# Optimization experiments

Measured on AMD Instinct MI355X. Metric: run time of the kernel, lower is better.

Reference implementation:

```python
import jax, jax.numpy as jnp
import numpy as np

B, N, D, C, H = 16384, 32, 256, 128, 8
LEAKY_ALPHA = 0.2  # tf.nn.leaky_relu default


def setup_inputs() -> dict:
    key = jax.random.key(0)
    k1, k2, k3, k4 = jax.random.split(key, 4)
    return {
        "node_feats": jax.random.normal(k1, (B, D), dtype=jnp.float32),
        "neighbors_feats": jax.random.normal(k2, (B, N, D), dtype=jnp.float32),
        "kernel": jax.random.normal(k3, (D, C), dtype=jnp.float32) * 0.05,
        "attn_kernel": jax.random.normal(k4, (1, H, 2 * C), dtype=jnp.float32) * 0.05,
        "attn_bias": jnp.zeros((H * C,), dtype=jnp.float32),
    }


def reference(node_feats, neighbors_feats, kernel, attn_kernel, attn_bias):
    # Project node and neighbor features: [B,C], [B,N,C]
    node_p = jnp.einsum('bd,dc->bc', node_feats, kernel)
    neigh_p = jnp.einsum('bnd,dc->bnc', neighbors_feats, kernel)
    # attn_kernel [1,H,2C]: split instead of materializing tile+concat [B,N,2C]
    a = attn_kernel[0]                 # [H, 2C]
    a_src, a_dst = a[:, :C], a[:, C:]  # each [H, C]
    # score[b,n,h] = concat(node_p[b], neigh_p[b,n]) . a[h]
    scores = (jnp.einsum('bc,hc->bh', node_p, a_src)[:, None, :]
              + jnp.einsum('bnc,hc->bnh', neigh_p, a_dst))  # [B,N,H]
    scores = jnp.transpose(scores, (0, 2, 1))  # [B,H,N]
    coef = jax.nn.softmax(jax.nn.leaky_relu(scores, LEAKY_ALPHA), axis=-1)
    # dropout is identity at inference (Keras default training=False)
    z = jnp.einsum('bhn,bnc->bhc', coef, neigh_p)  # [B,H,C]
    z = z.reshape(B, H * C) + attn_bias            # concat heads + bias
    return z[None, ...]  # [1,B,H*C]
```

## Files before the change

### kernel.cpp

```cpp
#include <hip/hip_runtime.h>

#define BB 16384
#define NN 32
#define DD 256
#define CC 128
#define HH 8
#define ALPHA 0.2f

#define SA_STRIDE 264
#define SP_STRIDE 48

typedef __attribute__((ext_vector_type(8))) short bf16x8;
typedef __attribute__((ext_vector_type(4))) float f32x4;

__device__ __forceinline__ unsigned short f2b(float x) {
    unsigned int u = __float_as_uint(x);
    return (unsigned short)((u + 0x7fffu + ((u >> 16) & 1u)) >> 16);
}
__device__ __forceinline__ uint2 pack4(float a, float b, float c, float d) {
    uint2 r;
    r.x = (unsigned)f2b(a) | ((unsigned)f2b(b) << 16);
    r.y = (unsigned)f2b(c) | ((unsigned)f2b(d) << 16);
    return r;
}

__global__ __launch_bounds__(256) void prep_kernel(const float* __restrict__ kern,
                                                   const float* __restrict__ attn,
                                                   unsigned short* __restrict__ kfrag,
                                                   unsigned short* __restrict__ sfrag) {
    if (blockIdx.x < 16) {
        int tid = blockIdx.x * 256 + threadIdx.x;
        int nt   = tid >> 9;
        int ks   = (tid >> 6) & 7;
        int lane = tid & 63;
        int q    = lane >> 4;
        int cc   = lane & 15;
        int c    = nt * 16 + cc;
        unsigned short v[8];
#pragma unroll
        for (int j = 0; j < 8; ++j) {
            int k = ks * 32 + q * 8 + j;
            v[j] = f2b(kern[k * CC + c]);
        }
        uint4* dst = (uint4*)(kfrag + ((size_t)(nt * 8 + ks) * 64 + lane) * 8);
        uint4 pk;
        pk.x = (unsigned)v[0] | ((unsigned)v[1] << 16);
        pk.y = (unsigned)v[2] | ((unsigned)v[3] << 16);
        pk.z = (unsigned)v[4] | ((unsigned)v[5] << 16);
        pk.w = (unsigned)v[6] | ((unsigned)v[7] << 16);
        *dst = pk;
    } else {
        int sid = (blockIdx.x - 16) * 256 + threadIdx.x;
        int ks   = sid >> 6;
        int lane = sid & 63;
        int q    = lane >> 4;
        int cc   = lane & 15;
        unsigned short v[8];
#pragma unroll
        for (int j = 0; j < 8; ++j) {
            int k = ks * 32 + q * 8 + j;
            const float* krow = kern + (size_t)k * CC;
            const float* arow = (cc < 8) ? (attn + cc * (2 * CC) + CC)
                                         : (attn + (cc - 8) * (2 * CC));
            float s0 = 0.f, s1 = 0.f;
#pragma unroll 4
            for (int c = 0; c < CC; c += 2) {
                s0 += krow[c] * arow[c];
                s1 += krow[c + 1] * arow[c + 1];
            }
            v[j] = f2b(s0 + s1);
        }
        uint4* dst = (uint4*)(sfrag + ((size_t)ks * 64 + lane) * 8);
        uint4 pk;
        pk.x = (unsigned)v[0] | ((unsigned)v[1] << 16);
        pk.y = (unsigned)v[2] | ((unsigned)v[3] << 16);
        pk.z = (unsigned)v[4] | ((unsigned)v[5] << 16);
        pk.w = (unsigned)v[6] | ((unsigned)v[7] << 16);
        *dst = pk;
    }
}

__global__ __launch_bounds__(256, 4) void gat_kernel(const float* __restrict__ node,
                                                     const float* __restrict__ neigh,
                                                     const float* __restrict__ bias,
                                                     const unsigned short* __restrict__ kfrag,
                                                     const unsigned short* __restrict__ sfrag,
                                                     float* __restrict__ out) {
    const int b    = blockIdx.x;
    const int t    = threadIdx.x;
    const int lane = t & 63;
    const int wave = t >> 6;
    const int q    = lane >> 4;
    const int m15  = lane & 15;

    __shared__ __align__(16) char smem[39712];
    unsigned short* sA    = (unsigned short*)smem;
    unsigned short* sP    = (unsigned short*)(smem + 25344);
    unsigned short* cfrag = (unsigned short*)(smem + 37632);
    float*          sDst  = (float*)(smem + 38656);
    float*          sSrc  = (float*)(smem + 39680);

    {
        const float4* nb4 = (const float4*)(neigh + (size_t)b * (NN * DD));
        const float4* nd4 = (const float4*)(node + (size_t)b * DD);
        for (int j = t; j < 33 * 64; j += 256) {
            int row = j >> 6, d4 = j & 63;
            float4 v = (row < 32) ? nb4[row * 64 + d4] : nd4[d4];
            *(uint2*)(sA + row * SA_STRIDE + d4 * 4) = pack4(v.x, v.y, v.z, v.w);
        }
    }
    __syncthreads();

    if (wave < 3) {
        const int mt = wave;
        f32x4 acc = {0.f, 0.f, 0.f, 0.f};
        const unsigned short* abase = sA + (mt * 16 + m15) * SA_STRIDE + q * 8;
#pragma unroll
        for (int ks = 0; ks < 8; ++ks) {
            bf16x8 bfr = *(const bf16x8*)(sfrag + ((size_t)ks * 64 + lane) * 8);
            bf16x8 afr = *(const bf16x8*)(abase + ks * 32);
            acc = __builtin_amdgcn_mfma_f32_16x16x32_bf16(afr, bfr, acc, 0, 0, 0);
        }
#pragma unroll
        for (int r = 0; r < 4; ++r) {
            int row = mt * 16 + q * 4 + r;
            if (row < 32 && m15 < 8) sDst[row * 8 + m15] = acc[r];
            if (row == 32 && m15 >= 8) sSrc[m15 - 8] = acc[r];
        }
    }

#pragma unroll
    for (int nti = 0; nti < 2; ++nti) {
        const int nt = wave * 2 + nti;
        bf16x8 kb[8];
#pragma unroll
        for (int ks = 0; ks < 8; ++ks)
            kb[ks] = *(const bf16x8*)(kfrag + ((size_t)(nt * 8 + ks) * 64 + lane) * 8);
#pragma unroll
        for (int mt = 0; mt < 2; ++mt) {
            f32x4 acc = {0.f, 0.f, 0.f, 0.f};
            const unsigned short* abase = sA + (mt * 16 + m15) * SA_STRIDE + q * 8;
#pragma unroll
            for (int ks = 0; ks < 8; ++ks) {
                bf16x8 afr = *(const bf16x8*)(abase + ks * 32);
                acc = __builtin_amdgcn_mfma_f32_16x16x32_bf16(afr, kb[ks], acc, 0, 0, 0);
            }
            int c  = nt * 16 + m15;
            int n0 = mt * 16 + q * 4;
            *(uint2*)(sP + c * SP_STRIDE + n0) = pack4(acc[0], acc[1], acc[2], acc[3]);
        }
    }
    __syncthreads();

    {
        int h = t >> 5, n = t & 31;
        float sc = sSrc[h] + sDst[n * 8 + h];
        sc = fmaxf(sc, ALPHA * sc);
        float m = sc;
#pragma unroll
        for (int off = 16; off >= 1; off >>= 1) m = fmaxf(m, __shfl_xor(m, off, 32));
        float e = expf(sc - m);
        float den = e;
#pragma unroll
        for (int off = 16; off >= 1; off >>= 1) den += __shfl_xor(den, off, 32);
        float coef = e / den;
        int l1 = (n >> 3) * 16 + h;
        int jj = n & 7;
        cfrag[l1 * 8 + jj] = f2b(coef);
        cfrag[(l1 + 8) * 8 + jj] = 0;
    }
    __syncthreads();

    {
        bf16x8 cb = *(const bf16x8*)(cfrag + (size_t)lane * 8);
        f32x4 zero = {0.f, 0.f, 0.f, 0.f};
#pragma unroll
        for (int i = 0; i < 2; ++i) {
            int mt5 = wave * 2 + i;
            bf16x8 afr = *(const bf16x8*)(sP + (mt5 * 16 + m15) * SP_STRIDE + q * 8);
            f32x4 acc = __builtin_amdgcn_mfma_f32_16x16x32_bf16(afr, cb, zero, 0, 0, 0);
            if (m15 < 8) {
                int h  = m15;
                int c0 = mt5 * 16 + q * 4;
                float4 bv = *(const float4*)(bias + h * CC + c0);
                float4 r;
                r.x = acc[0] + bv.x;
                r.y = acc[1] + bv.y;
                r.z = acc[2] + bv.z;
                r.w = acc[3] + bv.w;
                *(float4*)(out + (size_t)b * (HH * CC) + h * CC + c0) = r;
            }
        }
    }
}

extern "C" void kernel_launch(void* const* d_in, const int* in_sizes, int n_in,
                              void* d_out, int out_size, void* d_ws, size_t ws_size,
                              hipStream_t stream) {
    const float* node  = (const float*)d_in[0];
    const float* neigh = (const float*)d_in[1];
    const float* kern  = (const float*)d_in[2];
    const float* attn  = (const float*)d_in[3];
    const float* bias  = (const float*)d_in[4];
    float* out = (float*)d_out;

    unsigned short* kfrag = (unsigned short*)d_ws;
    unsigned short* sfrag = (unsigned short*)((char*)d_ws + 65536);

    hipLaunchKernelGGL(prep_kernel, dim3(18), dim3(256), 0, stream, kern, attn, kfrag, sfrag);
    hipLaunchKernelGGL(gat_kernel, dim3(BB), dim3(256), 0, stream,
                       node, neigh, bias, kfrag, sfrag, out);
}
```

Measured before the change: 793.4 us.

## Make GAT blocks persistent over 8 batch rows with register-prefetched next-row loads

Each block now processes 8 consecutive batch rows instead of one, cutting the grid from one block per row to 2048 blocks. The next row's neighbor and node features are loaded into registers while the current row's projection, softmax and aggregation run, then written to shared memory after the projection buffer is no longer needed. This hides global load latency behind compute and amortizes per-block setup. In exchange it uses 36 extra VGPRs for the prefetch, drops the 4-blocks-per-CU launch bound, gives fewer blocks to schedule, and adds a padding change to the sP stride.

```diff
diff --git a/kernel.cpp b/kernel.cpp
--- a/kernel.cpp
+++ b/kernel.cpp
@@ -7,8 +7,18 @@
 #define HH 8
 #define ALPHA 0.2f
 
+#define GRID 2048
+#define NPB 8
+
 #define SA_STRIDE 264
-#define SP_STRIDE 48
+#define SP_STRIDE 56
+#define SA_BYTES (33 * SA_STRIDE * 2)
+#define SP_BYTES (CC * SP_STRIDE * 2)
+#define OFF_SP   SA_BYTES
+#define OFF_CF   (OFF_SP + SP_BYTES)
+#define OFF_DST  (OFF_CF + 1024)
+#define OFF_SRC  (OFF_DST + 1024)
+#define SMEM_TOT (OFF_SRC + 32)
 
 typedef __attribute__((ext_vector_type(8))) short bf16x8;
 typedef __attribute__((ext_vector_type(4))) float f32x4;
@@ -80,117 +90,164 @@
     }
 }
 
-__global__ __launch_bounds__(256, 4) void gat_kernel(const float* __restrict__ node,
-                                                     const float* __restrict__ neigh,
-                                                     const float* __restrict__ bias,
-                                                     const unsigned short* __restrict__ kfrag,
-                                                     const unsigned short* __restrict__ sfrag,
-                                                     float* __restrict__ out) {
-    const int b    = blockIdx.x;
+__global__ __launch_bounds__(256) void gat_kernel(const float* __restrict__ node,
+                                                  const float* __restrict__ neigh,
+                                                  const float* __restrict__ bias,
+                                                  const unsigned short* __restrict__ kfrag,
+                                                  const unsigned short* __restrict__ sfrag,
+                                                  float* __restrict__ out) {
     const int t    = threadIdx.x;
     const int lane = t & 63;
     const int wave = t >> 6;
     const int q    = lane >> 4;
     const int m15  = lane & 15;
 
-    __shared__ __align__(16) char smem[39712];
+    __shared__ __align__(16) char smem[SMEM_TOT];
     unsigned short* sA    = (unsigned short*)smem;
-    unsigned short* sP    = (unsigned short*)(smem + 25344);
-    unsigned short* cfrag = (unsigned short*)(smem + 37632);
-    float*          sDst  = (float*)(smem + 38656);
-    float*          sSrc  = (float*)(smem + 39680);
+    unsigned short* sP    = (unsigned short*)(smem + OFF_SP);
+    unsigned short* cfrag = (unsigned short*)(smem + OFF_CF);
+    float*          sDst  = (float*)(smem + OFF_DST);
+    float*          sSrc  = (float*)(smem + OFF_SRC);
+
+    const int base = blockIdx.x * NPB;
 
     {
-        const float4* nb4 = (const float4*)(neigh + (size_t)b * (NN * DD));
-        const float4* nd4 = (const float4*)(node + (size_t)b * DD);
-        for (int j = t; j < 33 * 64; j += 256) {
-            int row = j >> 6, d4 = j & 63;
-            float4 v = (row < 32) ? nb4[row * 64 + d4] : nd4[d4];
-            *(uint2*)(sA + row * SA_STRIDE + d4 * 4) = pack4(v.x, v.y, v.z, v.w);
+        int h = t >> 5, n = t & 31;
+        int l1 = (n >> 3) * 16 + h;
+        cfrag[(l1 + 8) * 8 + (n & 7)] = 0;
+    }
+
+    float4 r[9];
+
+    {
+        const float4* nb4 = (const float4*)(neigh + (size_t)base * (NN * DD));
+        const float4* nd4 = (const float4*)(node + (size_t)base * DD);
+#pragma unroll
+        for (int u = 0; u < 9; ++u) {
+            int j = t + (u << 8);
+            if (j < 33 * 64) {
+                int row = j >> 6, d4 = j & 63;
+                r[u] = (row < 32) ? nb4[row * 64 + d4] : nd4[d4];
+            }
+        }
+#pragma unroll
+        for (int u = 0; u < 9; ++u) {
+            int j = t + (u << 8);
+            if (j < 33 * 64) {
+                int row = j >> 6, d4 = j & 63;
+                *(uint2*)(sA + row * SA_STRIDE + d4 * 4) = pack4(r[u].x, r[u].y, r[u].z, r[u].w);
+            }
         }
     }
     __syncthreads();
 
-    if (wave < 3) {
-        const int mt = wave;
-        f32x4 acc = {0.f, 0.f, 0.f, 0.f};
-        const unsigned short* abase = sA + (mt * 16 + m15) * SA_STRIDE + q * 8;
-#pragma unroll
-        for (int ks = 0; ks < 8; ++ks) {
-            bf16x8 bfr = *(const bf16x8*)(sfrag + ((size_t)ks * 64 + lane) * 8);
-            bf16x8 afr = *(const bf16x8*)(abase + ks * 32);
-            acc = __builtin_amdgcn_mfma_f32_16x16x32_bf16(afr, bfr, acc, 0, 0, 0);
-        }
-#pragma unroll
-        for (int r = 0; r < 4; ++r) {
-            int row = mt * 16 + q * 4 + r;
-            if (row < 32 && m15 < 8) sDst[row * 8 + m15] = acc[r];
-            if (row == 32 && m15 >= 8) sSrc[m15 - 8] = acc[r];
-        }
-    }
-
-#pragma unroll
-    for (int nti = 0; nti < 2; ++nti) {
-        const int nt = wave * 2 + nti;
-        bf16x8 kb[8];
-#pragma unroll
-        for (int ks = 0; ks < 8; ++ks)
-            kb[ks] = *(const bf16x8*)(kfrag + ((size_t)(nt * 8 + ks) * 64 + lane) * 8);
-#pragma unroll
-        for (int mt = 0; mt < 2; ++mt) {
+    for (int i = 0; i < NPB; ++i) {
+        const int b = base + i;
+
+        if (i + 1 < NPB) {
+            const float4* nb4 = (const float4*)(neigh + (size_t)(b + 1) * (NN * DD));
+            const float4* nd4 = (const float4*)(node + (size_t)(b + 1) * DD);
+#pragma unroll
+            for (int u = 0; u < 9; ++u) {
+                int j = t + (u << 8);
+                if (j < 33 * 64) {
+                    int row = j >> 6, d4 = j & 63;
+                    r[u] = (row < 32) ? nb4[row * 64 + d4] : nd4[d4];
+                }
+            }
+        }
+
+        if (wave < 3) {
+            const int mt = wave;
             f32x4 acc = {0.f, 0.f, 0.f, 0.f};
             const unsigned short* abase = sA + (mt * 16 + m15) * SA_STRIDE + q * 8;
 #pragma unroll
             for (int ks = 0; ks < 8; ++ks) {
+                bf16x8 bfr = *(const bf16x8*)(sfrag + ((size_t)ks * 64 + lane) * 8);
                 bf16x8 afr = *(const bf16x8*)(abase + ks * 32);
-                acc = __builtin_amdgcn_mfma_f32_16x16x32_bf16(afr, kb[ks], acc, 0, 0, 0);
-            }
-            int c  = nt * 16 + m15;
-            int n0 = mt * 16 + q * 4;
-            *(uint2*)(sP + c * SP_STRIDE + n0) = pack4(acc[0], acc[1], acc[2], acc[3]);
-        }
-    }
-    __syncthreads();
-
-    {
-        int h = t >> 5, n = t & 31;
-        float sc = sSrc[h] + sDst[n * 8 + h];
-        sc = fmaxf(sc, ALPHA * sc);
-        float m = sc;
-#pragma unroll
-        for (int off = 16; off >= 1; off >>= 1) m = fmaxf(m, __shfl_xor(m, off, 32));
-        float e = expf(sc - m);
-        float den = e;
-#pragma unroll
-        for (int off = 16; off >= 1; off >>= 1) den += __shfl_xor(den, off, 32);
-        float coef = e / den;
-        int l1 = (n >> 3) * 16 + h;
-        int jj = n & 7;
-        cfrag[l1 * 8 + jj] = f2b(coef);
-        cfrag[(l1 + 8) * 8 + jj] = 0;
-    }
-    __syncthreads();
-
-    {
-        bf16x8 cb = *(const bf16x8*)(cfrag + (size_t)lane * 8);
-        f32x4 zero = {0.f, 0.f, 0.f, 0.f};
-#pragma unroll
-        for (int i = 0; i < 2; ++i) {
-            int mt5 = wave * 2 + i;
-            bf16x8 afr = *(const bf16x8*)(sP + (mt5 * 16 + m15) * SP_STRIDE + q * 8);
-            f32x4 acc = __builtin_amdgcn_mfma_f32_16x16x32_bf16(afr, cb, zero, 0, 0, 0);
-            if (m15 < 8) {
-                int h  = m15;
-                int c0 = mt5 * 16 + q * 4;
-                float4 bv = *(const float4*)(bias + h * CC + c0);
-                float4 r;
-                r.x = acc[0] + bv.x;
-                r.y = acc[1] + bv.y;
-                r.z = acc[2] + bv.z;
-                r.w = acc[3] + bv.w;
-                *(float4*)(out + (size_t)b * (HH * CC) + h * CC + c0) = r;
-            }
-        }
+                acc = __builtin_amdgcn_mfma_f32_16x16x32_bf16(afr, bfr, acc, 0, 0, 0);
+            }
+#pragma unroll
+            for (int rr = 0; rr < 4; ++rr) {
+                int row = mt * 16 + q * 4 + rr;
+                if (row < 32 && m15 < 8) sDst[row * 8 + m15] = acc[rr];
+                if (row == 32 && m15 >= 8) sSrc[m15 - 8] = acc[rr];
+            }
+        }
+
+#pragma unroll
+        for (int nti = 0; nti < 2; ++nti) {
+            const int nt = wave * 2 + nti;
+            bf16x8 kb[8];
+#pragma unroll
+            for (int ks = 0; ks < 8; ++ks)
+                kb[ks] = *(const bf16x8*)(kfrag + ((size_t)(nt * 8 + ks) * 64 + lane) * 8);
+#pragma unroll
+            for (int mt = 0; mt < 2; ++mt) {
+                f32x4 acc = {0.f, 0.f, 0.f, 0.f};
+                const unsigned short* abase = sA + (mt * 16 + m15) * SA_STRIDE + q * 8;
+#pragma unroll
+                for (int ks = 0; ks < 8; ++ks) {
+                    bf16x8 afr = *(const bf16x8*)(abase + ks * 32);
+                    acc = __builtin_amdgcn_mfma_f32_16x16x32_bf16(afr, kb[ks], acc, 0, 0, 0);
+                }
+                int c  = nt * 16 + m15;
+                int n0 = mt * 16 + q * 4;
+                *(uint2*)(sP + c * SP_STRIDE + n0) = pack4(acc[0], acc[1], acc[2], acc[3]);
+            }
+        }
+        __syncthreads();
+
+        {
+            int h = t >> 5, n = t & 31;
+            float sc = sSrc[h] + sDst[n * 8 + h];
+            sc = fmaxf(sc, ALPHA * sc);
+            float m = sc;
+#pragma unroll
+            for (int off = 16; off >= 1; off >>= 1) m = fmaxf(m, __shfl_xor(m, off, 32));
+            float e = expf(sc - m);
+            float den = e;
+#pragma unroll
+            for (int off = 16; off >= 1; off >>= 1) den += __shfl_xor(den, off, 32);
+            float coef = e / den;
+            int l1 = (n >> 3) * 16 + h;
+            cfrag[l1 * 8 + (n & 7)] = f2b(coef);
+        }
+
+        if (i + 1 < NPB) {
+#pragma unroll
+            for (int u = 0; u < 9; ++u) {
+                int j = t + (u << 8);
+                if (j < 33 * 64) {
+                    int row = j >> 6, d4 = j & 63;
+                    *(uint2*)(sA + row * SA_STRIDE + d4 * 4) = pack4(r[u].x, r[u].y, r[u].z, r[u].w);
+                }
+            }
+        }
+        __syncthreads();
+
+        {
+            bf16x8 cb = *(const bf16x8*)(cfrag + (size_t)lane * 8);
+            f32x4 zero = {0.f, 0.f, 0.f, 0.f};
+#pragma unroll
+            for (int ii = 0; ii < 2; ++ii) {
+                int mt5 = wave * 2 + ii;
+                bf16x8 afr = *(const bf16x8*)(sP + (mt5 * 16 + m15) * SP_STRIDE + q * 8);
+                f32x4 acc = __builtin_amdgcn_mfma_f32_16x16x32_bf16(afr, cb, zero, 0, 0, 0);
+                if (m15 < 8) {
+                    int h  = m15;
+                    int c0 = mt5 * 16 + q * 4;
+                    float4 bv = *(const float4*)(bias + h * CC + c0);
+                    float4 rv;
+                    rv.x = acc[0] + bv.x;
+                    rv.y = acc[1] + bv.y;
+                    rv.z = acc[2] + bv.z;
+                    rv.w = acc[3] + bv.w;
+                    *(float4*)(out + (size_t)b * (HH * CC) + h * CC + c0) = rv;
+                }
+            }
+        }
+        __syncthreads();
     }
 }
 
@@ -208,6 +265,6 @@
     unsigned short* sfrag = (unsigned short*)((char*)d_ws + 65536);
 
     hipLaunchKernelGGL(prep_kernel, dim3(18), dim3(256), 0, stream, kern, attn, kfrag, sfrag);
-    hipLaunchKernelGGL(gat_kernel, dim3(BB), dim3(256), 0, stream,
+    hipLaunchKernelGGL(gat_kernel, dim3(GRID), dim3(256), 0, stream,
                        node, neigh, bias, kfrag, sfrag, out);
 }
```

Result: no change. 795.1 us (+0.2%).
